# Kernel optimization log

Hardware: AMD Instinct MI355X
Metric: run time of the kernel (lower is better)

Reference implementation:

```python
import jax, jax.numpy as jnp
import numpy as np

DIM = 1024
SEQ_LEN = 4096
K = 256
HEADS = 16
DIM_HEAD = DIM // HEADS  # 64
BATCH = 4


def setup_inputs() -> dict:
    key = jax.random.key(0)
    ks = jax.random.split(key, 8)
    x = jax.random.normal(ks[0], (BATCH, SEQ_LEN, DIM), dtype=jnp.float32)
    # nn.Linear weights are [out, in]; y = x @ W.T
    std_lin = 1.0 / np.sqrt(DIM)
    Wq = jax.random.uniform(ks[1], (HEADS * DIM_HEAD, DIM), minval=-std_lin, maxval=std_lin, dtype=jnp.float32)
    Wk = jax.random.uniform(ks[2], (HEADS * DIM_HEAD, DIM), minval=-std_lin, maxval=std_lin, dtype=jnp.float32)
    Wv = jax.random.uniform(ks[3], (HEADS * DIM_HEAD, DIM), minval=-std_lin, maxval=std_lin, dtype=jnp.float32)
    # proj_k/proj_v init_: uniform(-1/sqrt(k), 1/sqrt(k)) on [seq_len, k]
    std_p = 1.0 / np.sqrt(K)
    proj_k = jax.random.uniform(ks[4], (SEQ_LEN, K), minval=-std_p, maxval=std_p, dtype=jnp.float32)
    proj_v = jax.random.uniform(ks[5], (SEQ_LEN, K), minval=-std_p, maxval=std_p, dtype=jnp.float32)
    std_o = 1.0 / np.sqrt(HEADS * DIM_HEAD)
    Wo = jax.random.uniform(ks[6], (DIM, HEADS * DIM_HEAD), minval=-std_o, maxval=std_o, dtype=jnp.float32)
    bo = jax.random.uniform(ks[7], (DIM,), minval=-std_o, maxval=std_o, dtype=jnp.float32)
    return {"x": x, "Wq": Wq, "Wk": Wk, "Wv": Wv, "proj_k": proj_k, "proj_v": proj_v, "Wo": Wo, "bo": bo}


def reference(x, Wq, Wk, Wv, proj_k, proj_v, Wo, bo):
    b, n, d = x.shape
    h, dh, k = HEADS, DIM_HEAD, K
    # q/k/v projections
    q = jnp.einsum('bnd,ed->bne', x, Wq)            # [b, n, h*dh]
    keys = jnp.einsum('bnd,ed->bne', x, Wk)         # [b, n, h*dh]
    vals = jnp.einsum('bnd,ed->bne', x, Wv)         # [b, n, h*dh]
    # low-rank projection along sequence: [b, n, e] x [n, k] -> [b, k, e]
    keys = jnp.einsum('bne,nk->bke', keys, proj_k[:n])
    vals = jnp.einsum('bne,nk->bke', vals, proj_v[:n])
    # split heads
    q = q.reshape(b, n, h, dh).transpose(0, 2, 1, 3)        # [b, h, n, dh]
    keys = keys.reshape(b, k, h, dh).transpose(0, 2, 1, 3)  # [b, h, k, dh]
    vals = vals.reshape(b, k, h, dh).transpose(0, 2, 1, 3)  # [b, h, k, dh]
    dots = jnp.einsum('bhnd,bhkd->bhnk', q, keys) * (dh ** -0.5)
    attn = jax.nn.softmax(dots, axis=-1)
    out = jnp.einsum('bhnk,bhkd->bhnd', attn, vals)
    out = out.transpose(0, 2, 1, 3).reshape(b, n, h * dh)
    return jnp.einsum('bne,oe->bno', out, Wo) + bo
```

## Files before the change

kernel.cpp:

```cpp
#include <hip/hip_runtime.h>
#include <hip/hip_bf16.h>
#include <stdint.h>

typedef unsigned short u16;
typedef __attribute__((ext_vector_type(8))) short bf16x8;
typedef __attribute__((ext_vector_type(4))) float f32x4;

#define DEV __device__ __forceinline__

DEV u16 f2bf(float f) {
  union { float f; unsigned u; } v; v.f = f;
  unsigned r = (v.u + 0x7fffu + ((v.u >> 16) & 1u)) >> 16;
  return (u16)r;
}

DEV unsigned pk2(float lo, float hi) {
  union { __hip_bfloat162 h; unsigned u; } c;
  c.h = __float22bfloat162_rn(make_float2(lo, hi));
  return c.u;
}

DEV f32x4 mfma16(bf16x8 a, bf16x8 b, f32x4 c) {
  return __builtin_amdgcn_mfma_f32_16x16x32_bf16(a, b, c, 0, 0, 0);
}

DEV void gload_lds16(const u16* g, u16* l) {
  __builtin_amdgcn_global_load_lds((const __attribute__((address_space(1))) void*)g,
                                   (__attribute__((address_space(3))) void*)l, 16, 0, 0);
}

#define QSCALE 0.18033688011112042f

__global__ void cvt_xpose_kernel(const float* __restrict__ src, u16* __restrict__ dst_rm,
                                 u16* __restrict__ dst_tp, int R, int C,
                                 long zS, long zRM, long zTP) {
  __shared__ u16 tile[64][72];
  src += (size_t)blockIdx.z * zS;
  dst_tp += (size_t)blockIdx.z * zTP;
  int r0 = blockIdx.y * 64, c0 = blockIdx.x * 64;
  int tr = threadIdx.x >> 2, tc = (threadIdx.x & 3) * 16;
  const float* s = src + (size_t)(r0 + tr) * C + c0 + tc;
  u16 loc[16];
#pragma unroll
  for (int q = 0; q < 4; ++q) {
    float4 v = ((const float4*)s)[q];
    loc[q * 4 + 0] = f2bf(v.x); loc[q * 4 + 1] = f2bf(v.y);
    loc[q * 4 + 2] = f2bf(v.z); loc[q * 4 + 3] = f2bf(v.w);
  }
#pragma unroll
  for (int i = 0; i < 16; ++i) tile[tr][tc + i] = loc[i];
  if (dst_rm) {
    u16* d = dst_rm + (size_t)blockIdx.z * zRM + (size_t)(r0 + tr) * C + c0 + tc;
    *(bf16x8*)d = *(const bf16x8*)&loc[0];
    *(bf16x8*)(d + 8) = *(const bf16x8*)&loc[8];
  }
  __syncthreads();
  u16 tmp[16];
#pragma unroll
  for (int i = 0; i < 16; ++i) tmp[i] = tile[tc + i][tr];
  u16* d = dst_tp + (size_t)(c0 + tr) * R + r0 + tc;
  *(bf16x8*)d = *(const bf16x8*)&tmp[0];
  *(bf16x8*)(d + 8) = *(const bf16x8*)&tmp[8];
}

__global__ void cvt_w4_kernel(const float* __restrict__ s0, const float* __restrict__ s1,
                              const float* __restrict__ s2, const float* __restrict__ s3,
                              u16* __restrict__ d0, u16* __restrict__ d1,
                              u16* __restrict__ d2, u16* __restrict__ d3) {
  const float* s; u16* d;
  switch (blockIdx.y) {
    case 0: s = s0; d = d0; break;
    case 1: s = s1; d = d1; break;
    case 2: s = s2; d = d2; break;
    default: s = s3; d = d3; break;
  }
  int i = blockIdx.x * 256 + threadIdx.x;
  float4 v = ((const float4*)s)[i];
  ushort4 o; o.x = f2bf(v.x); o.y = f2bf(v.y); o.z = f2bf(v.z); o.w = f2bf(v.w);
  ((ushort4*)d)[i] = o;
}

__global__ void reduce4_kernel(const float* __restrict__ part, u16* __restrict__ out) {
  int i = blockIdx.x * 256 + threadIdx.x;
  const float4* p = (const float4*)part;
  float4 a = p[i], b = p[i + 524288], c = p[i + 1048576], d = p[i + 1572864];
  ushort4 o;
  o.x = f2bf(a.x + b.x + c.x + d.x);
  o.y = f2bf(a.y + b.y + c.y + d.y);
  o.z = f2bf(a.z + b.z + c.z + d.z);
  o.w = f2bf(a.w + b.w + c.w + d.w);
  ((ushort4*)out)[i] = o;
}

template<int OMODE>
__global__ __launch_bounds__(256, 4)
void gemm_bt_kernel(const u16* __restrict__ A, const u16* __restrict__ Bt,
                    const u16* __restrict__ Bt2, void* __restrict__ Cout,
                    u16* __restrict__ CoutT, const float* __restrict__ bias, float cscale,
                    int ldA, int ldB, int ldC, int Klen,
                    long zA, long zB, long zC, int bMod, long kChunkA, long kChunkB) {
  __shared__ __align__(16) u16 smA[2][128 * 32];
  __shared__ __align__(16) u16 smB[2][128 * 32];
  const int t = threadIdx.x;
  const int lane = t & 63, wave = t >> 6;
  const int wm = wave & 1, wn = wave >> 1;
  const int g = lane >> 4, r = lane & 15;
  const int id = blockIdx.y * gridDim.x + blockIdx.x;
  const int cpx = (gridDim.x * gridDim.y) >> 3;
  const int s = (id & 7) * cpx + (id >> 3);
  const int bx = s % gridDim.x, by = s / gridDim.x;
  const int z = blockIdx.z;
  const int b = z % bMod, kc = z / bMod;
  const u16* Ab = A + (size_t)b * zA + (size_t)kc * kChunkA;
  const u16* Bbase = (Bt2 && (b & 1)) ? Bt2 : Bt;
  const u16* Bb = Bbase + (size_t)b * zB + (size_t)kc * kChunkB;
  const int m0 = by * 128, n0 = bx * 128;
  const int srow = t >> 2;
  const int lslot = ((t & 3) + 4 - ((srow >> 1) & 3)) & 3;

  f32x4 acc[4][4];
#pragma unroll
  for (int m = 0; m < 4; ++m)
#pragma unroll
    for (int n = 0; n < 4; ++n) acc[m][n] = f32x4{0.f, 0.f, 0.f, 0.f};

  auto STAGE = [&](int buf, int k0) {
#pragma unroll
    for (int p = 0; p < 2; ++p) {
      int row = p * 64 + srow;
      gload_lds16(Ab + (size_t)(m0 + row) * ldA + k0 + lslot * 8, &smA[buf][p * 2048 + wave * 512]);
      gload_lds16(Bb + (size_t)(n0 + row) * ldB + k0 + lslot * 8, &smB[buf][p * 2048 + wave * 512]);
    }
  };

  const int nt = Klen >> 5;
  STAGE(0, 0);
  __syncthreads();
  int cur = 0;
  for (int it = 0; it < nt; ++it) {
    if (it + 1 < nt) STAGE(cur ^ 1, (it + 1) << 5);
    bf16x8 af[4], bfr[4];
#pragma unroll
    for (int m = 0; m < 4; ++m) {
      int row = wm * 64 + m * 16 + r;
      int ps = (g + (row >> 1)) & 3;
      af[m] = *(const bf16x8*)&smA[cur][row * 32 + ps * 8];
    }
#pragma unroll
    for (int n = 0; n < 4; ++n) {
      int row = wn * 64 + n * 16 + r;
      int ps = (g + (row >> 1)) & 3;
      bfr[n] = *(const bf16x8*)&smB[cur][row * 32 + ps * 8];
    }
#pragma unroll
    for (int m = 0; m < 4; ++m)
#pragma unroll
      for (int n = 0; n < 4; ++n)
        acc[m][n] = mfma16(af[m], bfr[n], acc[m][n]);
    __syncthreads();
    cur ^= 1;
  }

  if constexpr (OMODE == 0) {
    u16* C = (u16*)Cout + (size_t)z * zC;
#pragma unroll
    for (int n = 0; n < 4; ++n) {
      int col = n0 + wn * 64 + n * 16 + r;
#pragma unroll
      for (int m = 0; m < 4; ++m) {
        int rowb = m0 + wm * 64 + m * 16 + 4 * g;
#pragma unroll
        for (int rr = 0; rr < 4; ++rr)
          C[(size_t)(rowb + rr) * ldC + col] = f2bf(acc[m][n][rr] * cscale);
      }
    }
  } else if constexpr (OMODE == 2) {
    float* myF = ((float*)(wave < 2 ? (void*)&smA[0][0] : (void*)&smB[0][0])) + (wave & 1) * 2048;
    float* Cg = (float*)Cout + (size_t)z * zC + (size_t)(m0 + wm * 64) * ldC + n0 + wn * 64;
#pragma unroll
    for (int np = 0; np < 2; ++np) {
#pragma unroll
      for (int n2 = 0; n2 < 2; ++n2)
#pragma unroll
        for (int m = 0; m < 4; ++m)
#pragma unroll
          for (int rr = 0; rr < 4; ++rr) {
            int rl = m * 16 + 4 * g + rr;
            int cl = n2 * 16 + r;
            myF[rl * 32 + ((((cl >> 2) ^ (rl & 7)) & 7) << 2) + (cl & 3)] =
                acc[m][np * 2 + n2][rr];
          }
      __syncthreads();
#pragma unroll
      for (int i = 0; i < 8; ++i) {
        int idx = i * 64 + lane;
        int row = idx >> 3, c = idx & 7;
        float4 v = *(const float4*)&myF[row * 32 + (((c ^ (row & 7)) & 7) << 2)];
        *(float4*)&Cg[(size_t)row * ldC + np * 32 + c * 4] = v;
      }
      __syncthreads();
    }
  } else if constexpr (OMODE == 3) {
    if ((z & 1) == 0) {
      u16* C = (u16*)Cout + (size_t)(z >> 1) * zC;
#pragma unroll
      for (int n = 0; n < 4; ++n) {
        int col = n0 + wn * 64 + n * 16 + r;
#pragma unroll
        for (int m = 0; m < 4; ++m) {
          int rowb = m0 + wm * 64 + m * 16 + 4 * g;
#pragma unroll
          for (int rr = 0; rr < 4; ++rr)
            C[(size_t)(rowb + rr) * ldC + col] = f2bf(acc[m][n][rr]);
        }
      }
    } else {
      u16* C = CoutT + (size_t)(z >> 1) * zC;
#pragma unroll
      for (int n = 0; n < 4; ++n) {
        int col = n0 + wn * 64 + n * 16 + r;
#pragma unroll
        for (int m = 0; m < 4; ++m) {
          int rowb = m0 + wm * 64 + m * 16 + 4 * g;
          ushort4 o;
          o.x = f2bf(acc[m][n][0]); o.y = f2bf(acc[m][n][1]);
          o.z = f2bf(acc[m][n][2]); o.w = f2bf(acc[m][n][3]);
          *(ushort4*)&C[(size_t)col * 256 + rowb] = o;
        }
      }
    }
  } else {
    float* C = (float*)Cout + (size_t)z * zC;
#pragma unroll
    for (int n = 0; n < 4; ++n) {
      int col = n0 + wn * 64 + n * 16 + r;
      float bv = (OMODE == 1) ? bias[col] : 0.f;
#pragma unroll
      for (int m = 0; m < 4; ++m) {
        int rowb = m0 + wm * 64 + m * 16 + 4 * g;
#pragma unroll
        for (int rr = 0; rr < 4; ++rr)
          C[(size_t)(rowb + rr) * ldC + col] = acc[m][n][rr] + bv;
      }
    }
  }
}

#define MFMA_CLUSTER(MH, NH, AF, BV)                                                    \
  do {                                                                                  \
    __builtin_amdgcn_s_setprio(1);                                                      \
    _Pragma("unroll")                                                                   \
    for (int mi = 0; mi < 4; ++mi)                                                      \
      _Pragma("unroll")                                                                 \
      for (int ni = 0; ni < 2; ++ni) {                                                  \
        acc[(MH)*4+mi][(NH)*2+ni] = mfma16(AF[mi][0], BV[ni][0], acc[(MH)*4+mi][(NH)*2+ni]); \
        acc[(MH)*4+mi][(NH)*2+ni] = mfma16(AF[mi][1], BV[ni][1], acc[(MH)*4+mi][(NH)*2+ni]); \
      }                                                                                 \
    __builtin_amdgcn_s_setprio(0);                                                      \
  } while (0)

#define ENDBAR(W)                                                                       \
  do {                                                                                  \
    if ((W) == 1) asm volatile("s_waitcnt vmcnt(4)" ::: "memory");                      \
    if ((W) == 2) asm volatile("s_waitcnt vmcnt(0)" ::: "memory");                      \
    __builtin_amdgcn_s_barrier();                                                       \
  } while (0)

template<int OMODE>
__global__ __launch_bounds__(512, 1)
void gemm256_kernel(const u16* __restrict__ A, const u16* __restrict__ Bt,
                    void* __restrict__ Cout, const float* __restrict__ bias,
                    float cscale, int ldA, int ldB, int ldC, int Klen) {
  __shared__ __align__(16) u16 lds[65536];
  const int t = threadIdx.x;
  const int lane = t & 63, wave = t >> 6;
  const int g = lane >> 4, r = lane & 15, rm = r & 7;
  const int wm = wave >> 2, wn = wave & 3;
  const int id = blockIdx.y * 4 + blockIdx.x;
  const int sw = (id & 7) * 32 + (id >> 3);
  const int bx = sw & 3, by = sw >> 2;
  const int m0 = by * 256, n0 = bx * 256;

  const int trow = t >> 3, tslot = t & 7;
  const int sslot = tslot ^ (trow & 7);
  const u16* Asrc = A + (size_t)(m0 + trow) * ldA + sslot * 8;
  const u16* Bsrc = Bt + sslot * 8;
  const int bRow0 = n0 + (trow >> 5) * 64 + (trow & 31);
  const int bRow1 = n0 + (2 + (trow >> 5)) * 64 + (trow & 31);

  u16* const A0 = lds;
  u16* const A1 = lds + 16384;
  u16* const B0 = lds + 32768;
  u16* const B1 = lds + 49152;

  auto stageA = [&](u16* buf, int h, int k0) {
    u16* d = buf + h * 8192 + t * 8;
    const u16* s0 = Asrc + (size_t)(h * 64) * ldA + k0;
    gload_lds16(s0, d);
    gload_lds16(s0 + (size_t)128 * ldA, d + 4096);
  };
  auto stageB = [&](u16* buf, int h, int k0) {
    u16* d = buf + h * 8192 + t * 8;
    gload_lds16(Bsrc + (size_t)(bRow0 + h * 32) * ldB + k0, d);
    gload_lds16(Bsrc + (size_t)(bRow1 + h * 32) * ldB + k0, d + 4096);
  };

  const int aoff = wm * 64 + r;
  const int boff = wn * 32 + r;

  auto loadA = [&](bf16x8 af[4][2], const u16* base, int MH) {
#pragma unroll
    for (int mi = 0; mi < 4; ++mi) {
      const u16* rp = base + (MH * 128 + aoff + mi * 16) * 64;
      af[mi][0] = *(const bf16x8*)&rp[(g ^ rm) * 8];
      af[mi][1] = *(const bf16x8*)&rp[((4 + g) ^ rm) * 8];
    }
  };
  auto loadB = [&](bf16x8 bv[2][2], const u16* base, int NH) {
#pragma unroll
    for (int ni = 0; ni < 2; ++ni) {
      const u16* rp = base + (NH * 128 + boff + ni * 16) * 64;
      bv[ni][0] = *(const bf16x8*)&rp[(g ^ rm) * 8];
      bv[ni][1] = *(const bf16x8*)&rp[((4 + g) ^ rm) * 8];
    }
  };

  f32x4 acc[8][4];
#pragma unroll
  for (int m = 0; m < 8; ++m)
#pragma unroll
    for (int n = 0; n < 4; ++n) acc[m][n] = f32x4{0.f, 0.f, 0.f, 0.f};

  stageA(A0, 0, 0); stageB(B0, 0, 0); stageA(A0, 1, 0); stageB(B0, 1, 0);
  stageA(A1, 0, 64); stageB(B1, 0, 64);
  asm volatile("s_waitcnt vmcnt(4)" ::: "memory");
  __builtin_amdgcn_s_barrier();

  const int nt = Klen >> 6;
  for (int j = 0; j < (nt >> 1); ++j) {
    const int ta = 2 * j, tb = ta + 1;
    const int more = (ta + 2 < nt);
    const int kb = tb * 64, kn = (ta + 2) * 64, kn2 = (tb + 2) * 64;
    bf16x8 af[4][2], bv0[2][2], bv1[2][2];
    loadA(af, A0, 0); loadB(bv0, B0, 0);
    stageA(A1, 1, kb);
    MFMA_CLUSTER(0, 0, af, bv0); ENDBAR(0);
    loadB(bv1, B0, 1);
    stageB(B1, 1, kb);
    MFMA_CLUSTER(0, 1, af, bv1); ENDBAR(0);
    loadA(af, A0, 1);
    if (more) stageA(A0, 0, kn);
    MFMA_CLUSTER(1, 0, af, bv0); ENDBAR(0);
    if (more) stageB(B0, 0, kn);
    MFMA_CLUSTER(1, 1, af, bv1); ENDBAR(more ? 1 : 2);
    loadA(af, A1, 0); loadB(bv0, B1, 0);
    if (more) stageA(A0, 1, kn);
    MFMA_CLUSTER(0, 0, af, bv0); ENDBAR(0);
    loadB(bv1, B1, 1);
    if (more) stageB(B0, 1, kn);
    MFMA_CLUSTER(0, 1, af, bv1); ENDBAR(0);
    loadA(af, A1, 1);
    if (more) stageA(A1, 0, kn2);
    MFMA_CLUSTER(1, 0, af, bv0); ENDBAR(0);
    if (more) stageB(B1, 0, kn2);
    MFMA_CLUSTER(1, 1, af, bv1); ENDBAR(more ? 1 : 2);
  }

  if constexpr (OMODE == 0) {
    u16* myT = lds + wave * 8192;
#pragma unroll
    for (int m = 0; m < 8; ++m)
#pragma unroll
      for (int n = 0; n < 4; ++n)
#pragma unroll
        for (int rr = 0; rr < 4; ++rr) {
          int rl = m * 16 + 4 * g + rr;
          int cl = n * 16 + r;
          myT[rl * 64 + (((cl >> 3) ^ (rl & 7)) << 3) + (cl & 7)] = f2bf(acc[m][n][rr] * cscale);
        }
    u16* Cg = (u16*)Cout + (size_t)(m0 + wm * 128) * ldC + n0 + wn * 64;
#pragma unroll
    for (int i = 0; i < 16; ++i) {
      int idx = i * 64 + lane;
      int row = idx >> 3, c8 = idx & 7;
      bf16x8 v = *(const bf16x8*)&myT[row * 64 + ((c8 ^ (row & 7)) << 3)];
      *(bf16x8*)&Cg[(size_t)row * ldC + c8 * 8] = v;
    }
  } else {
    float* myF = (float*)lds + wave * 4096;
    float bvn[4];
#pragma unroll
    for (int n = 0; n < 4; ++n) bvn[n] = bias[n0 + wn * 64 + n * 16 + r];
    float* Cg = (float*)Cout + (size_t)(m0 + wm * 128) * ldC + n0 + wn * 64;
#pragma unroll
    for (int half = 0; half < 2; ++half) {
#pragma unroll
      for (int m2 = 0; m2 < 4; ++m2)
#pragma unroll
        for (int n = 0; n < 4; ++n)
#pragma unroll
          for (int rr = 0; rr < 4; ++rr) {
            int rl = m2 * 16 + 4 * g + rr;
            int cl = n * 16 + r;
            myF[rl * 64 + (((cl >> 2) ^ (rl & 15)) << 2) + (cl & 3)] =
                acc[half * 4 + m2][n][rr] + bvn[n];
          }
#pragma unroll
      for (int i = 0; i < 16; ++i) {
        int idx = i * 64 + lane;
        int row = idx >> 4, c4 = idx & 15;
        float4 v = *(const float4*)&myF[row * 64 + ((c4 ^ (row & 15)) << 2)];
        *(float4*)&Cg[(size_t)(half * 64 + row) * ldC + c4 * 4] = v;
      }
    }
  }
}

__global__ __launch_bounds__(256, 3)
void attn_kernel(const u16* __restrict__ Q, const u16* __restrict__ Kl,
                 const u16* __restrict__ VT, u16* __restrict__ Out) {
  __shared__ __align__(16) u16 sm[24576];
  const int t = threadIdx.x, lane = t & 63, w = t >> 6;
  const int g = lane >> 4, r = lane & 15;
  const int id = (blockIdx.y << 6) | blockIdx.x;
  const int s = (id & 7) * (gridDim.y << 3) + (id >> 3);
  const int b = blockIdx.z, h = s >> 6, n0 = (s & 63) * 64;
  const u16* Kb = Kl + (size_t)b * 262144 + h * 64;
  const u16* Vb = VT + (size_t)b * 262144 + (size_t)(h * 64) * 256;
  u16* vbase = sm + 16384;

  const int vd = t >> 2;
  const int vsl = (t & 3) ^ (vd & 3);
  auto stage_slice = [&](int kk) {
    gload_lds16(Vb + (size_t)vd * 256 + kk * 32 + vsl * 8,
                vbase + (kk & 3) * 2048 + w * 512);
  };

#pragma unroll
  for (int p = 0; p < 8; ++p) {
    int row = p * 32 + (t >> 3);
    int ls = ((t & 7) + 8 - (row & 7)) & 7;
    gload_lds16(Kb + (size_t)row * 1024 + ls * 8, sm + p * 2048 + w * 512);
  }
#pragma unroll
  for (int kk = 0; kk < 4; ++kk) stage_slice(kk);
  const int qrow = n0 + w * 16 + r;
  const u16* Qp = Q + ((size_t)(b * 4096 + qrow)) * 1024 + h * 64 + g * 8;
  bf16x8 aq0 = *(const bf16x8*)Qp;
  bf16x8 aq1 = *(const bf16x8*)(Qp + 32);
  asm volatile("s_waitcnt vmcnt(4)" ::: "memory");
  __builtin_amdgcn_s_barrier();

  f32x4 dotv[16];
  __builtin_amdgcn_s_setprio(1);
#pragma unroll
  for (int kf = 0; kf < 16; ++kf) {
    int row = kf * 16 + r;
    bf16x8 kb0 = *(const bf16x8*)&sm[row * 64 + ((g + row) & 7) * 8];
    bf16x8 kb1 = *(const bf16x8*)&sm[row * 64 + ((4 + g + row) & 7) * 8];
    f32x4 d = f32x4{0.f, 0.f, 0.f, 0.f};
    d = mfma16(kb0, aq0, d);
    d = mfma16(kb1, aq1, d);
    dotv[kf] = d;
  }
  __builtin_amdgcn_s_setprio(0);
  asm volatile("s_waitcnt vmcnt(3)" ::: "memory");
  __builtin_amdgcn_s_barrier();

  float mx = -3.4e38f;
#pragma unroll
  for (int kf = 0; kf < 16; ++kf)
    mx = fmaxf(mx, fmaxf(fmaxf(dotv[kf][0], dotv[kf][1]), fmaxf(dotv[kf][2], dotv[kf][3])));
  mx = fmaxf(mx, __shfl_xor(mx, 16, 64));
  mx = fmaxf(mx, __shfl_xor(mx, 32, 64));
  float ssum = 0.f;
#pragma unroll
  for (int kf = 0; kf < 16; ++kf)
#pragma unroll
    for (int j = 0; j < 4; ++j) {
      float p = __builtin_amdgcn_exp2f(dotv[kf][j] - mx);
      dotv[kf][j] = p;
      ssum += p;
    }
  ssum += __shfl_xor(ssum, 16, 64);
  ssum += __shfl_xor(ssum, 32, 64);
  const float inv = 1.f / ssum;
  float invv[4];
#pragma unroll
  for (int rr = 0; rr < 4; ++rr) invv[rr] = __shfl(inv, 4 * g + rr, 64);

  const int q16 = w * 16 + r;
  const int qx = (q16 & 7) << 3;
#pragma unroll
  for (int kf = 0; kf < 16; ++kf) {
    uint2 val;
    val.x = pk2(dotv[kf][0], dotv[kf][1]);
    val.y = pk2(dotv[kf][2], dotv[kf][3]);
    *(uint2*)&sm[(q16 * 256 + kf * 16 + 4 * g) ^ qx] = val;
  }

  f32x4 oacc[4];
#pragma unroll
  for (int df = 0; df < 4; ++df) oacc[df] = f32x4{0.f, 0.f, 0.f, 0.f};
#pragma unroll
  for (int kk = 0; kk < 8; ++kk) {
    bf16x8 ap = *(const bf16x8*)&sm[(q16 * 256 + kk * 32 + g * 8) ^ qx];
    const u16* vb = vbase + (kk & 3) * 2048;
    __builtin_amdgcn_s_setprio(1);
#pragma unroll
    for (int df = 0; df < 4; ++df) {
      int d = df * 16 + r;
      bf16x8 bv = *(const bf16x8*)&vb[d * 32 + (g ^ (d & 3)) * 8];
      oacc[df] = mfma16(ap, bv, oacc[df]);
    }
    __builtin_amdgcn_s_setprio(0);
    if (kk < 7) {
      if (kk < 5)       asm volatile("s_waitcnt vmcnt(2)" ::: "memory");
      else if (kk == 5) asm volatile("s_waitcnt vmcnt(1)" ::: "memory");
      else              asm volatile("s_waitcnt vmcnt(0)" ::: "memory");
      __builtin_amdgcn_s_barrier();
      if (kk < 4) stage_slice(kk + 4);
    }
  }

  u16* myO = sm + w * 4096;
#pragma unroll
  for (int df = 0; df < 4; ++df)
#pragma unroll
    for (int rr = 0; rr < 4; ++rr) {
      int row = 4 * g + rr;
      int col = df * 16 + r;
      myO[row * 64 + (((col >> 3) ^ (row & 7)) << 3) + (col & 7)] = f2bf(oacc[df][rr] * invv[rr]);
    }
#pragma unroll
  for (int i = 0; i < 2; ++i) {
    int idx = i * 64 + lane;
    int row = idx >> 3, c8 = idx & 7;
    bf16x8 v = *(const bf16x8*)&myO[row * 64 + ((c8 ^ (row & 7)) << 3)];
    *(bf16x8*)&Out[((size_t)(b * 4096 + n0 + w * 16 + row)) * 1024 + h * 64 + c8 * 8] = v;
  }
}

extern "C" void kernel_launch(void* const* d_in, const int* in_sizes, int n_in,
                              void* d_out, int out_size, void* d_ws, size_t ws_size,
                              hipStream_t stream) {
  const float* x  = (const float*)d_in[0];
  const float* Wq = (const float*)d_in[1];
  const float* Wk = (const float*)d_in[2];
  const float* Wv = (const float*)d_in[3];
  const float* pk = (const float*)d_in[4];
  const float* pv = (const float*)d_in[5];
  const float* Wo = (const float*)d_in[6];
  const float* bo = (const float*)d_in[7];

  u16* ws = (u16*)d_ws;
  u16* xbf   = ws;
  u16* xT    = xbf + 16777216;
  u16* wqb   = xT + 16777216;
  u16* wkb   = wqb + 1048576;
  u16* wvb   = wkb + 1048576;
  u16* wob   = wvb + 1048576;
  u16* projT = wob + 1048576;
  u16* Qb    = projT + 2097152;
  u16* xp    = Qb + 16777216;
  u16* klow  = xp + 2097152;
  u16* vT    = klow + 1048576;
  u16* aout  = xbf;
  float* xp_part = (float*)Qb;

  cvt_xpose_kernel<<<dim3(16, 64, 4), 256, 0, stream>>>(x, xbf, xT, 4096, 1024,
                                                        4194304, 4194304, 4194304);
  cvt_w4_kernel<<<dim3(1024, 4), 256, 0, stream>>>(Wq, Wk, Wv, Wo, wqb, wkb, wvb, wob);
  cvt_xpose_kernel<<<dim3(4, 64, 1), 256, 0, stream>>>(pk, nullptr, projT, 4096, 256, 0, 0, 0);
  cvt_xpose_kernel<<<dim3(4, 64, 1), 256, 0, stream>>>(pv, nullptr, projT + 1048576, 4096, 256, 0, 0, 0);
  gemm_bt_kernel<2><<<dim3(32, 4, 4), 256, 0, stream>>>(
      projT, xT, nullptr, (void*)xp_part, nullptr, nullptr, 1.f,
      4096, 4096, 4096, 1024, 0, 0, 2097152, 1, 1024, 1024);
  reduce4_kernel<<<2048, 256, 0, stream>>>(xp_part, xp);
  gemm_bt_kernel<3><<<dim3(8, 2, 8), 256, 0, stream>>>(
      xp, wkb, wvb, (void*)klow, vT, nullptr, 1.f,
      4096, 1024, 1024, 1024, 1048576, 0, 262144, 2, 1024, 0);
  gemm256_kernel<0><<<dim3(4, 64), 512, 0, stream>>>(
      xbf, wqb, (void*)Qb, nullptr, QSCALE, 1024, 1024, 1024, 1024);
  attn_kernel<<<dim3(64, 16, 4), 256, 0, stream>>>(Qb, klow, vT, aout);
  gemm256_kernel<1><<<dim3(4, 64), 512, 0, stream>>>(
      aout, wob, d_out, bo, 1.f, 1024, 1024, 1024, 1024);
}
```

Before: 212.4 us.

## Replace Q projection GEMM with 128x256-tile kernel and LDS-staged stores

Adds a dedicated Q-projection GEMM that uses 128x256 output tiles with 512 threads, double-buffered direct-to-LDS loads with a swizzled layout, and a launch bound of 4 blocks per CU. The grid doubles to 512 blocks, which should fill the CUs better than the 256-tile kernel. Block IDs are remapped to group neighbouring tiles. The epilogue writes the scaled bf16 output through a swizzled LDS transpose so global stores are 16-byte and coalesced. The smaller tile raises reuse overhead per output and uses a simpler single-K-step pipeline than the previous kernel.

```diff
diff --git a/kernel.cpp b/kernel.cpp
--- a/kernel.cpp
+++ b/kernel.cpp
@@ -242,6 +242,96 @@
         for (int rr = 0; rr < 4; ++rr)
           C[(size_t)(rowb + rr) * ldC + col] = acc[m][n][rr] + bv;
       }
+    }
+  }
+}
+
+__global__ __launch_bounds__(512, 4)
+void qgemm128_kernel(const u16* __restrict__ A, const u16* __restrict__ Bt,
+                     u16* __restrict__ Cout, float cscale,
+                     int ldA, int ldB, int ldC, int Klen) {
+  __shared__ __align__(16) u16 lds[24576];
+  const int t = threadIdx.x;
+  const int lane = t & 63, wave = t >> 6;
+  const int g = lane >> 4, r = lane & 15;
+  const int wm = wave >> 2, wn = wave & 3;
+  const int id = blockIdx.y * gridDim.x + blockIdx.x;
+  const int cpx = (gridDim.x * gridDim.y) >> 3;
+  const int s = (id & 7) * cpx + (id >> 3);
+  const int bx = s & 3, by = s >> 2;
+  const int m0 = by * 128, n0 = bx * 256;
+
+  const int srow = t >> 2;
+  const int lslot = ((t & 3) + 4 - ((srow >> 1) & 3)) & 3;
+
+  auto STAGE = [&](int buf, int k0) {
+    gload_lds16(A + (size_t)(m0 + srow) * ldA + k0 + lslot * 8,
+                lds + buf * 4096 + t * 8);
+#pragma unroll
+    for (int p = 0; p < 2; ++p)
+      gload_lds16(Bt + (size_t)(n0 + p * 128 + srow) * ldB + k0 + lslot * 8,
+                  lds + 8192 + buf * 8192 + p * 4096 + t * 8);
+  };
+
+  f32x4 acc[4][4];
+#pragma unroll
+  for (int m = 0; m < 4; ++m)
+#pragma unroll
+    for (int n = 0; n < 4; ++n) acc[m][n] = f32x4{0.f, 0.f, 0.f, 0.f};
+
+  const int nt = Klen >> 5;
+  STAGE(0, 0);
+  __syncthreads();
+  int cur = 0;
+  for (int it = 0; it < nt; ++it) {
+    if (it + 1 < nt) STAGE(cur ^ 1, (it + 1) << 5);
+    const u16* Ab = lds + cur * 4096;
+    const u16* Bb = lds + 8192 + cur * 8192;
+    bf16x8 af[4], bfr[4];
+#pragma unroll
+    for (int m = 0; m < 4; ++m) {
+      int row = wm * 64 + m * 16 + r;
+      int ps = (g + (row >> 1)) & 3;
+      af[m] = *(const bf16x8*)&Ab[row * 32 + ps * 8];
+    }
+#pragma unroll
+    for (int n = 0; n < 4; ++n) {
+      int row = wn * 64 + n * 16 + r;
+      int ps = (g + (row >> 1)) & 3;
+      bfr[n] = *(const bf16x8*)&Bb[row * 32 + ps * 8];
+    }
+    __builtin_amdgcn_s_setprio(1);
+#pragma unroll
+    for (int m = 0; m < 4; ++m)
+#pragma unroll
+      for (int n = 0; n < 4; ++n)
+        acc[m][n] = mfma16(af[m], bfr[n], acc[m][n]);
+    __builtin_amdgcn_s_setprio(0);
+    __syncthreads();
+    cur ^= 1;
+  }
+
+  u16* myT = lds + wave * 2048;
+  u16* Cg = Cout + (size_t)(m0 + wm * 64) * ldC + n0 + wn * 64;
+#pragma unroll
+  for (int np = 0; np < 2; ++np) {
+#pragma unroll
+    for (int n2 = 0; n2 < 2; ++n2)
+#pragma unroll
+      for (int m = 0; m < 4; ++m)
+#pragma unroll
+        for (int rr = 0; rr < 4; ++rr) {
+          int rl = m * 16 + 4 * g + rr;
+          int cl = n2 * 16 + r;
+          myT[rl * 32 + (((cl >> 3) ^ (rl & 3)) << 3) + (cl & 7)] =
+              f2bf(acc[m][np * 2 + n2][rr] * cscale);
+        }
+#pragma unroll
+    for (int i = 0; i < 4; ++i) {
+      int idx = i * 64 + lane;
+      int row = idx >> 2, c = idx & 3;
+      bf16x8 v = *(const bf16x8*)&myT[row * 32 + ((c ^ (row & 3)) << 3)];
+      *(bf16x8*)&Cg[(size_t)row * ldC + np * 32 + c * 8] = v;
     }
   }
 }
@@ -580,8 +670,8 @@
   gemm_bt_kernel<3><<<dim3(8, 2, 8), 256, 0, stream>>>(
       xp, wkb, wvb, (void*)klow, vT, nullptr, 1.f,
       4096, 1024, 1024, 1024, 1048576, 0, 262144, 2, 1024, 0);
-  gemm256_kernel<0><<<dim3(4, 64), 512, 0, stream>>>(
-      xbf, wqb, (void*)Qb, nullptr, QSCALE, 1024, 1024, 1024, 1024);
+  qgemm128_kernel<<<dim3(4, 128), 512, 0, stream>>>(
+      xbf, wqb, Qb, QSCALE, 1024, 1024, 1024, 1024);
   attn_kernel<<<dim3(64, 16, 4), 256, 0, stream>>>(Qb, klow, vT, aout);
   gemm256_kernel<1><<<dim3(4, 64), 512, 0, stream>>>(
       aout, wob, d_out, bo, 1.f, 1024, 1024, 1024, 1024);
```

New measurement: 213.2 us. Within noise of the previous version (+0.4%).
